# Optimization experiments

Measured on AMD Instinct MI355X. Metric: run time of the kernel, lower is better.

Reference implementation:

```python
import jax, jax.numpy as jnp
import numpy as np

B = 32          # decode batch
H = 32          # query heads (TP shard)
KV_LORA = 512   # latent dim
ROPE = 64       # rope head dim
NOPE = 128      # nope head dim
VH = 128        # v head dim
QL = 1536       # q lora rank
HID = 5120      # model hidden
BLK = 128       # page/block size
BLOCKS_PER_SEQ = 32   # 4096-token context
NB = B * BLOCKS_PER_SEQ
CACHE_BLOCKS = 1200


def _rope(x, pos):
    # x: [B, n, ROPE] (neox half-rotation), pos: [B] int positions
    half = x.shape[-1] // 2
    inv = 1.0 / (10000.0 ** (jnp.arange(half, dtype=jnp.float32) / half))
    ang = pos.astype(jnp.float32)[:, None] * inv              # [B, half]
    cos, sin = jnp.cos(ang)[:, None, :], jnp.sin(ang)[:, None, :]
    x1, x2 = x[..., :half], x[..., half:]
    return jnp.concatenate([x1 * cos - x2 * sin, x2 * cos + x1 * sin], axis=-1)


def setup_inputs() -> dict:
    key = jax.random.key(0)
    ks = jax.random.split(key, 10)
    inp = {
        'hidden_states_or_q_c': jax.random.normal(ks[0], (B, QL), jnp.float32),
        'k_c_normed': jax.random.normal(ks[1], (B, 1, KV_LORA), jnp.float32),
        'k_pe': jax.random.normal(ks[2], (B, 1, ROPE), jnp.float32),
        'kv_cache_k': jax.random.normal(ks[3], (CACHE_BLOCKS, BLK, ROPE), jnp.float32),
        'kv_cache_v': jax.random.normal(ks[4], (CACHE_BLOCKS, BLK, KV_LORA), jnp.float32),
        'W_Q': jax.random.normal(ks[5], (QL, H * NOPE), jnp.float32) / np.sqrt(QL),
        'W_UK': jax.random.normal(ks[6], (H, NOPE, KV_LORA), jnp.float32) / np.sqrt(NOPE),
        'W_QR': jax.random.normal(ks[7], (QL, H * ROPE), jnp.float32) / np.sqrt(QL),
        'W_UV': jax.random.normal(ks[8], (H, KV_LORA, VH), jnp.float32) / np.sqrt(KV_LORA),
        'W_O': jax.random.normal(ks[9], (H * VH, HID), jnp.float32) / np.sqrt(H * VH),
        'input_positions': jnp.full((B,), BLK * BLOCKS_PER_SEQ - 1, jnp.int32),
        'block_list': jnp.arange(NB, dtype=jnp.int32),
        'block_groups': (jnp.arange(NB, dtype=jnp.int32) // BLOCKS_PER_SEQ),
        'block_bias': jnp.zeros((NB, BLK), jnp.float32),
        'block_indices': (jnp.arange(B, dtype=jnp.int32) * BLOCKS_PER_SEQ + BLOCKS_PER_SEQ - 1),
        'block_offsets': jnp.full((B,), BLK - 1, jnp.int32),
    }
    inp['block_mapping'] = jax.nn.one_hot(inp['block_groups'], B, dtype=jnp.float32)
    return inp


def reference(hidden_states_or_q_c, k_c_normed, k_pe, kv_cache_k, kv_cache_v,
              W_Q, W_UK, W_QR, W_UV, W_O,
              input_positions, block_list, block_groups, block_mapping,
              block_bias, block_indices, block_offsets):
    b = hidden_states_or_q_c.shape[0]
    h, nope, kv_lora = W_UK.shape
    rope = k_pe.shape[-1]
    scale = 1.0 / np.sqrt(nope + rope)

    # absorbed q projection: q_nope in latent space (_q_proj_and_k_up_proj)
    q_nope = jnp.einsum('bq,qhd->bhd', hidden_states_or_q_c, W_Q.reshape(-1, h, nope))
    q_nope = jnp.einsum('bhd,hdl->bhl', q_nope, W_UK)          # [B,H,kv_lora]
    q_pe = (hidden_states_or_q_c @ W_QR).reshape(b, h, rope)
    pos = input_positions.reshape(b)
    q_pe = _rope(q_pe, pos)
    k_pe_r = _rope(k_pe, pos)                                  # [B,1,rope]

    # write new latent token into paged cache (latent_cache_k / latent_cache_v)
    kv_cache_k = kv_cache_k.at[block_indices, block_offsets].set(k_pe_r[:, 0, :])
    kv_cache_v = kv_cache_v.at[block_indices, block_offsets].set(k_c_normed[:, 0, :])

    # flat_pa_mla: query [B,H,kv_lora+rope], key = concat(value_latent, k_pe)
    q = jnp.concatenate([q_nope, q_pe], axis=-1) * scale       # [B,H,576]
    keys = kv_cache_k[block_list]                              # [NB,BLK,rope]
    vals = kv_cache_v[block_list]                              # [NB,BLK,kv_lora]
    kcat = jnp.concatenate([vals, keys], axis=-1)              # [NB,BLK,576]

    qb = jnp.einsum('nb,bhd->nhd', block_mapping, q)           # batch2block
    logits = jnp.einsum('nhd,nkd->nhk', qb, kcat) + block_bias[:, None, :]

    # grouped (per-batch) softmax across this batch's blocks == pipelined_pa math
    gmax = jax.ops.segment_max(logits.max(-1), block_groups, num_segments=b)  # [B,H]
    p = jnp.exp(logits - gmax[block_groups][:, :, None])       # [NB,H,BLK]
    av = jnp.einsum('nhk,nkl->nhl', p, vals)                   # [NB,H,kv_lora]
    num = jnp.einsum('nb,nhl->bhl', block_mapping, av)         # block2batch
    den = jnp.einsum('nb,nh->bh', block_mapping, p.sum(-1))
    attn = num / den[..., None]                                # [B,H,kv_lora]

    # _v_up_proj_and_o_proj
    out = jnp.einsum('bhl,hlv->bhv', attn, W_UV).reshape(b, -1) @ W_O
    return out.reshape(b, 1, -1)
```

## Files before the change

kernel.cpp:

```cpp
#include <hip/hip_runtime.h>
#include <hip/hip_bf16.h>
#include <stdint.h>


typedef __attribute__((ext_vector_type(8))) short short8;
typedef __attribute__((ext_vector_type(4))) float f32x4;

__device__ inline uint32_t f2bf(float f) {
  uint32_t u = __float_as_uint(f);
  return (u + 0x7fffu + ((u >> 16) & 1u)) >> 16;
}
union Bf2U { __hip_bfloat162 h; uint32_t u; };
__device__ inline uint32_t pack2bf(float lo, float hi) {
  Bf2U v; v.h = __float22bfloat162_rn(float2{lo, hi});
  return v.u;
}
union FragU { uint32_t u[4]; short8 s; };
__device__ inline short8 frag_from(const uint32_t r[4]) {
  FragU v; v.u[0] = r[0]; v.u[1] = r[1]; v.u[2] = r[2]; v.u[3] = r[3];
  return v.s;
}

__global__ __launch_bounds__(256) void k1_qproj(
    const float* __restrict__ hidden, const float* __restrict__ W_Q,
    const float* __restrict__ W_QR, float* __restrict__ q_nope0,
    float* __restrict__ q_pe0) {
  __shared__ float hl[32][129];
  const int t = threadIdx.x;
  const int ctile = blockIdx.x * 128;
  const int k0 = blockIdx.y * 128;
  const bool isQ = (ctile < 4096);
  const float* W = isQ ? W_Q : W_QR;
  const int wstride = isQ ? 4096 : 2048;
  const int c = (isQ ? ctile : ctile - 4096) + (t & 31) * 4;
  const int rg = t >> 5;
  for (int idx = t; idx < 4096; idx += 256) {
    int b = idx >> 7, kk = idx & 127;
    hl[b][kk] = hidden[b * 1536 + k0 + kk];
  }
  __syncthreads();
  float acc[4][4];
#pragma unroll
  for (int r = 0; r < 4; ++r)
#pragma unroll
    for (int j = 0; j < 4; ++j) acc[r][j] = 0.f;
  const float* wp = W + (size_t)k0 * wstride + c;
#pragma unroll 4
  for (int kk = 0; kk < 128; ++kk) {
    float4 w = *(const float4*)wp;
    wp += wstride;
#pragma unroll
    for (int r = 0; r < 4; ++r) {
      float hv = hl[rg * 4 + r][kk];
      acc[r][0] += hv * w.x;
      acc[r][1] += hv * w.y;
      acc[r][2] += hv * w.z;
      acc[r][3] += hv * w.w;
    }
  }
  float* dst = isQ ? q_nope0 : q_pe0;
#pragma unroll
  for (int r = 0; r < 4; ++r)
#pragma unroll
    for (int j = 0; j < 4; ++j)
      atomicAdd(&dst[(rg * 4 + r) * wstride + c + j], acc[r][j]);
}

__global__ __launch_bounds__(256) void k2_qlora(
    const float* __restrict__ q_nope0, const float* __restrict__ W_UK,
    float* __restrict__ q_acc) {
  __shared__ float qn[32][33];
  const int t = threadIdx.x;
  const int h = blockIdx.y;
  const int c0 = blockIdx.x * 128;
  const int d0 = blockIdx.z * 32;
  for (int idx = t; idx < 1024; idx += 256) {
    int b = idx >> 5, dd = idx & 31;
    qn[b][dd] = q_nope0[b * 4096 + h * 128 + d0 + dd];
  }
  __syncthreads();
  const int c = c0 + (t & 31) * 4;
  const int rg = t >> 5;
  float acc[4][4];
#pragma unroll
  for (int r = 0; r < 4; ++r)
#pragma unroll
    for (int j = 0; j < 4; ++j) acc[r][j] = 0.f;
  const float* wp = W_UK + (size_t)(h * 128 + d0) * 512 + c;
#pragma unroll 4
  for (int dd = 0; dd < 32; ++dd) {
    float4 w = *(const float4*)wp;
    wp += 512;
#pragma unroll
    for (int r = 0; r < 4; ++r) {
      float qv = qn[rg * 4 + r][dd];
      acc[r][0] += qv * w.x;
      acc[r][1] += qv * w.y;
      acc[r][2] += qv * w.z;
      acc[r][3] += qv * w.w;
    }
  }
#pragma unroll
  for (int r = 0; r < 4; ++r)
#pragma unroll
    for (int j = 0; j < 4; ++j)
      atomicAdd(&q_acc[(size_t)((rg * 4 + r) * 32 + h) * 512 + c + j],
                acc[r][j]);
}

__global__ __launch_bounds__(256) void k2b_rope_scatter(
    const float* __restrict__ q_pe0, const float* __restrict__ k_pe,
    const float* __restrict__ k_c_normed, const int* __restrict__ ipos,
    const int* __restrict__ bindices, const int* __restrict__ boffsets,
    const float* __restrict__ q_acc, float* __restrict__ cache_k,
    float* __restrict__ cache_v, uint16_t* __restrict__ q_bf) {
  const int b = blockIdx.x;
  const int hs = blockIdx.y * 4;
  const int t = threadIdx.x;
  const float pos = (float)ipos[b];
  const float scale = 0.07216878364870323f;
  const float lnk = 0.28782313662425575f;
  for (int idx = t; idx < 2048; idx += 256) {
    int h = hs + (idx >> 9), c = idx & 511;
    q_bf[((size_t)b * 32 + h) * 576 + c] =
        (uint16_t)f2bf(q_acc[((size_t)b * 32 + h) * 512 + c] * scale);
  }
  if (t < 128) {
    int h = hs + (t >> 5), i = t & 31;
    float ang = pos * __expf(-(float)i * lnk);
    float s, c;
    sincosf(ang, &s, &c);
    float x1 = q_pe0[b * 2048 + h * 64 + i];
    float x2 = q_pe0[b * 2048 + h * 64 + 32 + i];
    int base = (b * 32 + h) * 576 + 512;
    q_bf[base + i]      = (uint16_t)f2bf((x1 * c - x2 * s) * scale);
    q_bf[base + 32 + i] = (uint16_t)f2bf((x2 * c + x1 * s) * scale);
  }
  if (blockIdx.y == 0) {
    const int row = bindices[b] * 128 + boffsets[b];
    if (t < 32) {
      int i = t;
      float ang = pos * __expf(-(float)i * lnk);
      float s, c;
      sincosf(ang, &s, &c);
      float x1 = k_pe[b * 64 + i], x2 = k_pe[b * 64 + 32 + i];
      cache_k[row * 64 + i]      = x1 * c - x2 * s;
      cache_k[row * 64 + 32 + i] = x2 * c + x1 * s;
    }
    for (int j = t; j < 512; j += 256)
      cache_v[row * 512 + j] = k_c_normed[b * 512 + j];
  }
}

__global__ __launch_bounds__(256, 2) void k3_attn(
    const uint16_t* __restrict__ q_bf, const float* __restrict__ cache_k,
    const float* __restrict__ cache_v, const int* __restrict__ block_list,
    const int* __restrict__ block_groups, const float* __restrict__ block_bias,
    float* __restrict__ num_part, float* __restrict__ den_part) {
  __shared__ uint32_t Tl[288 * 33];
  __shared__ uint32_t Pl[16 * 33];
  __shared__ float den_sh[2][32];

  const int t = threadIdx.x;
  const int part = blockIdx.x, bseq = blockIdx.y;
  const int wg = bseq * 16 + part;
  const int wave = t >> 6, lane = t & 63, quad = lane >> 4, l16 = lane & 15;
  const int hh = wave >> 1, kvh = wave & 1;
  const int n0 = bseq * 32 + part * 2;
  const int g = block_groups[n0];

  uint32_t qf[72];
  {
    const uint32_t* qrow =
        (const uint32_t*)(q_bf + (size_t)(g * 32 + hh * 16 + l16) * 576);
#pragma unroll
    for (int ks = 0; ks < 18; ++ks)
#pragma unroll
      for (int i = 0; i < 4; ++i)
        qf[ks * 4 + i] = qrow[ks * 16 + quad * 4 + i];
  }

  const f32x4 fzero = {0.f, 0.f, 0.f, 0.f};
  f32x4 acc[2][8];
#pragma unroll
  for (int mt = 0; mt < 2; ++mt)
#pragma unroll
    for (int nt = 0; nt < 8; ++nt) acc[mt][nt] = fzero;
  float den_acc[4] = {0.f, 0.f, 0.f, 0.f};

  for (int blk_i = 0; blk_i < 2; ++blk_i) {
    const int n = n0 + blk_i;
    const int phys = block_list[n];
    const float* vrow = cache_v + (size_t)phys * 128 * 512;
    const float* krow = cache_k + (size_t)phys * 128 * 64;
    for (int s = 0; s < 4; ++s) {
      const int s0 = s * 32;
      __syncthreads();
      for (int idx = t; idx < 4608; idx += 256) {
        int kv = idx / 144, f4 = idx - kv * 144;
        float4 v; int d0;
        if (f4 < 128) { v = *(const float4*)(vrow + (s0 + kv) * 512 + f4 * 4); d0 = f4 * 4; }
        else { v = *(const float4*)(krow + (s0 + kv) * 64 + (f4 - 128) * 4); d0 = 512 + (f4 - 128) * 4; }
        int d2 = d0 >> 1;
        Tl[(d2    ) * 33 + kv] = pack2bf(v.x, v.y);
        Tl[(d2 + 1) * 33 + kv] = pack2bf(v.z, v.w);
      }
      __syncthreads();
      const int tkv = kvh * 16 + l16;
      f32x4 lg = fzero;
#pragma unroll
      for (int ks = 0; ks < 18; ++ks) {
        uint32_t br[4];
#pragma unroll
        for (int i = 0; i < 4; ++i)
          br[i] = Tl[(ks * 16 + quad * 4 + i) * 33 + tkv];
        lg = __builtin_amdgcn_mfma_f32_16x16x32_bf16(
            frag_from(&qf[ks * 4]), frag_from(br), lg, 0, 0, 0);
      }
      float bias = block_bias[n * 128 + s0 + tkv];
      uint32_t pb[4];
#pragma unroll
      for (int r = 0; r < 4; ++r) {
        float p = __expf(lg[r] + bias);
        pb[r] = f2bf(p);
        den_acc[r] += __uint_as_float(pb[r] << 16);
      }
#pragma unroll
      for (int r = 0; r < 4; ++r) {
        uint32_t other = (uint32_t)__shfl_xor((int)pb[r], 1, 64);
        if ((l16 & 1) == 0) {
          int h = hh * 16 + quad * 4 + r;
          Pl[(tkv >> 1) * 33 + h] = pb[r] | (other << 16);
        }
      }
      __syncthreads();
      uint32_t af[2][4];
#pragma unroll
      for (int mt = 0; mt < 2; ++mt)
#pragma unroll
        for (int i = 0; i < 4; ++i)
          af[mt][i] = Pl[(quad * 4 + i) * 33 + mt * 16 + l16];
#pragma unroll
      for (int nt = 0; nt < 8; ++nt) {
        int l = wave * 128 + nt * 16 + l16;
        const uint32_t* base = &Tl[(l >> 1) * 33 + quad * 8];
        uint32_t dw[8];
#pragma unroll
        for (int j = 0; j < 8; ++j) dw[j] = base[j];
        uint32_t br[4];
        const bool odd = (l & 1);
#pragma unroll
        for (int i = 0; i < 4; ++i) {
          uint32_t a = dw[2 * i], bq = dw[2 * i + 1];
          uint32_t lo = odd ? (a >> 16) : (a & 0xffffu);
          uint32_t hi = odd ? (bq & 0xffff0000u) : (bq << 16);
          br[i] = lo | hi;
        }
        short8 bf = frag_from(br);
        acc[0][nt] = __builtin_amdgcn_mfma_f32_16x16x32_bf16(
            frag_from(af[0]), bf, acc[0][nt], 0, 0, 0);
        acc[1][nt] = __builtin_amdgcn_mfma_f32_16x16x32_bf16(
            frag_from(af[1]), bf, acc[1][nt], 0, 0, 0);
      }
    }
  }
#pragma unroll
  for (int mt = 0; mt < 2; ++mt)
#pragma unroll
    for (int nt = 0; nt < 8; ++nt)
#pragma unroll
      for (int r = 0; r < 4; ++r) {
        int h = mt * 16 + quad * 4 + r;
        int l = wave * 128 + nt * 16 + l16;
        num_part[((size_t)wg * 32 + h) * 512 + l] = acc[mt][nt][r];
      }
  float dv[4];
#pragma unroll
  for (int r = 0; r < 4; ++r) {
    float v = den_acc[r];
    v += __shfl_xor(v, 1, 64);
    v += __shfl_xor(v, 2, 64);
    v += __shfl_xor(v, 4, 64);
    v += __shfl_xor(v, 8, 64);
    dv[r] = v;
  }
  if (l16 == 0) {
#pragma unroll
    for (int r = 0; r < 4; ++r)
      den_sh[kvh][hh * 16 + quad * 4 + r] = dv[r];
  }
  __syncthreads();
  if (t < 32) den_part[wg * 32 + t] = den_sh[0][t] + den_sh[1][t];
}

__global__ __launch_bounds__(256) void k4_reduce_wuv(
    const float* __restrict__ num_part, const float* __restrict__ den_part,
    const float* __restrict__ W_UV, float* __restrict__ o_acc) {
  __shared__ float attn[32][33];
  __shared__ float den[32];
  const int t = threadIdx.x;
  const int lc = blockIdx.x, h = blockIdx.y;
  const int c0 = lc * 32;
  if (t < 32) {
    float s = 0.f;
    for (int p = 0; p < 16; ++p) s += den_part[(t * 16 + p) * 32 + h];
    den[t] = s;
  }
  __syncthreads();
  {
    const int b = t >> 3, l4 = (t & 7) * 4;
    float4 s = {0.f, 0.f, 0.f, 0.f};
#pragma unroll
    for (int p = 0; p < 16; ++p) {
      float4 v = *(const float4*)&num_part[((size_t)(b * 16 + p) * 32 + h) * 512 + c0 + l4];
      s.x += v.x; s.y += v.y; s.z += v.z; s.w += v.w;
    }
    float inv = 1.f / den[b];
    attn[b][l4 + 0] = s.x * inv;
    attn[b][l4 + 1] = s.y * inv;
    attn[b][l4 + 2] = s.z * inv;
    attn[b][l4 + 3] = s.w * inv;
  }
  __syncthreads();
  const int v = t & 127, rg = t >> 7;
  float acc[16];
#pragma unroll
  for (int r = 0; r < 16; ++r) acc[r] = 0.f;
  for (int l = 0; l < 32; ++l) {
    float w = W_UV[(h * 512 + c0 + l) * 128 + v];
#pragma unroll
    for (int r = 0; r < 16; ++r) acc[r] += attn[rg * 16 + r][l] * w;
  }
  for (int r = 0; r < 16; ++r)
    atomicAdd(&o_acc[(size_t)(rg * 16 + r) * 4096 + h * 128 + v], acc[r]);
}

__global__ __launch_bounds__(256) void k5_wo(
    const float* __restrict__ o_acc, const float* __restrict__ W_O,
    float* __restrict__ out) {
  __shared__ uint32_t Bt[32 * 130];
  const int t = threadIdx.x;
  const int ksplit = blockIdx.x, ntile = blockIdx.y;
  const int n0 = ntile * 128, kbase = ksplit * 256;
  const int wave = t >> 6, lane = t & 63, quad = lane >> 4, l16 = lane & 15;
  const f32x4 fzero = {0.f, 0.f, 0.f, 0.f};
  f32x4 acc[2][2];
#pragma unroll
  for (int mt = 0; mt < 2; ++mt)
#pragma unroll
    for (int nt = 0; nt < 2; ++nt) acc[mt][nt] = fzero;
  for (int kc = 0; kc < 4; ++kc) {
    const int k0 = kbase + kc * 64;
    __syncthreads();
    for (int idx = t; idx < 1024; idx += 256) {
      int k2 = idx >> 5, c4 = idx & 31;
      const float* p0 = &W_O[(size_t)(k0 + 2 * k2) * 5120 + n0 + c4 * 4];
      float4 a = *(const float4*)p0;
      float4 b = *(const float4*)(p0 + 5120);
      uint32_t* bp = &Bt[k2 * 130 + c4 * 4];
      bp[0] = pack2bf(a.x, b.x);
      bp[1] = pack2bf(a.y, b.y);
      bp[2] = pack2bf(a.z, b.z);
      bp[3] = pack2bf(a.w, b.w);
    }
    __syncthreads();
#pragma unroll
    for (int ks2 = 0; ks2 < 2; ++ks2) {
      uint32_t af[2][4];
#pragma unroll
      for (int mt = 0; mt < 2; ++mt) {
        const float* orow =
            o_acc + (size_t)(mt * 16 + l16) * 4096 + k0 + ks2 * 32 + quad * 8;
        float4 x = *(const float4*)orow;
        float4 y = *(const float4*)(orow + 4);
        af[mt][0] = pack2bf(x.x, x.y);
        af[mt][1] = pack2bf(x.z, x.w);
        af[mt][2] = pack2bf(y.x, y.y);
        af[mt][3] = pack2bf(y.z, y.w);
      }
#pragma unroll
      for (int nt = 0; nt < 2; ++nt) {
        uint32_t br[4];
#pragma unroll
        for (int i = 0; i < 4; ++i)
          br[i] = Bt[(ks2 * 16 + quad * 4 + i) * 130 + wave * 32 + nt * 16 + l16];
        short8 bf = frag_from(br);
        acc[0][nt] = __builtin_amdgcn_mfma_f32_16x16x32_bf16(
            frag_from(af[0]), bf, acc[0][nt], 0, 0, 0);
        acc[1][nt] = __builtin_amdgcn_mfma_f32_16x16x32_bf16(
            frag_from(af[1]), bf, acc[1][nt], 0, 0, 0);
      }
    }
  }
#pragma unroll
  for (int mt = 0; mt < 2; ++mt)
#pragma unroll
    for (int nt = 0; nt < 2; ++nt)
#pragma unroll
      for (int r = 0; r < 4; ++r) {
        int b = mt * 16 + quad * 4 + r;
        int c = n0 + wave * 32 + nt * 16 + l16;
        atomicAdd(&out[(size_t)b * 5120 + c], acc[mt][nt][r]);
      }
}

extern "C" void kernel_launch(void* const* d_in, const int* in_sizes, int n_in,
                              void* d_out, int out_size, void* d_ws,
                              size_t ws_size, hipStream_t stream) {
  (void)in_sizes; (void)n_in; (void)ws_size;
  const float* hidden = (const float*)d_in[0];
  const float* k_c    = (const float*)d_in[1];
  const float* k_pe   = (const float*)d_in[2];
  float* cache_k      = (float*)d_in[3];
  float* cache_v      = (float*)d_in[4];
  const float* W_Q    = (const float*)d_in[5];
  const float* W_UK   = (const float*)d_in[6];
  const float* W_QR   = (const float*)d_in[7];
  const float* W_UV   = (const float*)d_in[8];
  const float* W_O    = (const float*)d_in[9];
  const int* ipos     = (const int*)d_in[10];
  const int* blist    = (const int*)d_in[11];
  const int* bgroups  = (const int*)d_in[12];
  const float* bbias  = (const float*)d_in[13];
  const int* bindices = (const int*)d_in[14];
  const int* boffsets = (const int*)d_in[15];

  char* ws = (char*)d_ws;
  float*    q_nope0  = (float*)(ws);
  float*    q_pe0    = (float*)(ws + 524288);
  float*    o_acc    = (float*)(ws + 786432);
  uint16_t* q_bf     = (uint16_t*)(ws + 1310720);
  float*    den_part = (float*)(ws + 2490368);
  float*    num_part = (float*)(ws + 2555904);
  float*    q_acc    = num_part;
  float*    out      = (float*)d_out;

  hipMemsetAsync(ws, 0, 1310720, stream);
  hipMemsetAsync((void*)q_acc, 0, 2097152, stream);
  hipMemsetAsync(d_out, 0, (size_t)out_size * sizeof(float), stream);

  k1_qproj<<<dim3(48, 12), 256, 0, stream>>>(hidden, W_Q, W_QR, q_nope0, q_pe0);
  k2_qlora<<<dim3(4, 32, 4), 256, 0, stream>>>(q_nope0, W_UK, q_acc);
  k2b_rope_scatter<<<dim3(32, 8), 256, 0, stream>>>(q_pe0, k_pe, k_c, ipos,
                                                    bindices, boffsets, q_acc,
                                                    cache_k, cache_v, q_bf);
  k3_attn<<<dim3(16, 32), 256, 0, stream>>>(q_bf, cache_k, cache_v, blist,
                                            bgroups, bbias, num_part, den_part);
  k4_reduce_wuv<<<dim3(16, 32), 256, 0, stream>>>(num_part, den_part, W_UV, o_acc);
  k5_wo<<<dim3(16, 40), 256, 0, stream>>>(o_acc, W_O, out);
}
```

Baseline: 702.4 us.

## Reduce attention partials with atomics and split cache tile loads

The attention kernel now adds its per-block numerator and denominator directly into per-sequence accumulators with atomicAdd, instead of writing 16 partials per sequence for the reduce kernel to sum. The reduce kernel only normalizes and applies W_UV, using 64-column tiles over half as many workgroups. The cache tile load loop is split into separate unrolled V and K loops, which removes the per-element branch and the division by 144. In exchange there is a larger memset, contention on the float atomics, and a floating-point summation order that is no longer deterministic.

```diff
diff --git a/kernel.cpp b/kernel.cpp
--- a/kernel.cpp
+++ b/kernel.cpp
@@ -156,14 +156,13 @@
     const uint16_t* __restrict__ q_bf, const float* __restrict__ cache_k,
     const float* __restrict__ cache_v, const int* __restrict__ block_list,
     const int* __restrict__ block_groups, const float* __restrict__ block_bias,
-    float* __restrict__ num_part, float* __restrict__ den_part) {
+    float* __restrict__ num_acc, float* __restrict__ den_acc) {
   __shared__ uint32_t Tl[288 * 33];
   __shared__ uint32_t Pl[16 * 33];
   __shared__ float den_sh[2][32];
 
   const int t = threadIdx.x;
   const int part = blockIdx.x, bseq = blockIdx.y;
-  const int wg = bseq * 16 + part;
   const int wave = t >> 6, lane = t & 63, quad = lane >> 4, l16 = lane & 15;
   const int hh = wave >> 1, kvh = wave & 1;
   const int n0 = bseq * 32 + part * 2;
@@ -186,7 +185,7 @@
   for (int mt = 0; mt < 2; ++mt)
 #pragma unroll
     for (int nt = 0; nt < 8; ++nt) acc[mt][nt] = fzero;
-  float den_acc[4] = {0.f, 0.f, 0.f, 0.f};
+  float den_acc_r[4] = {0.f, 0.f, 0.f, 0.f};
 
   for (int blk_i = 0; blk_i < 2; ++blk_i) {
     const int n = n0 + blk_i;
@@ -196,12 +195,21 @@
     for (int s = 0; s < 4; ++s) {
       const int s0 = s * 32;
       __syncthreads();
-      for (int idx = t; idx < 4608; idx += 256) {
-        int kv = idx / 144, f4 = idx - kv * 144;
-        float4 v; int d0;
-        if (f4 < 128) { v = *(const float4*)(vrow + (s0 + kv) * 512 + f4 * 4); d0 = f4 * 4; }
-        else { v = *(const float4*)(krow + (s0 + kv) * 64 + (f4 - 128) * 4); d0 = 512 + (f4 - 128) * 4; }
-        int d2 = d0 >> 1;
+#pragma unroll
+      for (int i = 0; i < 16; ++i) {
+        int idx = i * 256 + t;
+        int kv = idx >> 7, f4 = idx & 127;
+        float4 v = *(const float4*)(vrow + (s0 + kv) * 512 + f4 * 4);
+        int d2 = f4 * 2;
+        Tl[(d2    ) * 33 + kv] = pack2bf(v.x, v.y);
+        Tl[(d2 + 1) * 33 + kv] = pack2bf(v.z, v.w);
+      }
+#pragma unroll
+      for (int i = 0; i < 2; ++i) {
+        int idx = i * 256 + t;
+        int kv = idx >> 4, f4 = idx & 15;
+        float4 v = *(const float4*)(krow + (s0 + kv) * 64 + f4 * 4);
+        int d2 = 256 + f4 * 2;
         Tl[(d2    ) * 33 + kv] = pack2bf(v.x, v.y);
         Tl[(d2 + 1) * 33 + kv] = pack2bf(v.z, v.w);
       }
@@ -223,7 +231,7 @@
       for (int r = 0; r < 4; ++r) {
         float p = __expf(lg[r] + bias);
         pb[r] = f2bf(p);
-        den_acc[r] += __uint_as_float(pb[r] << 16);
+        den_acc_r[r] += __uint_as_float(pb[r] << 16);
       }
 #pragma unroll
       for (int r = 0; r < 4; ++r) {
@@ -272,12 +280,12 @@
       for (int r = 0; r < 4; ++r) {
         int h = mt * 16 + quad * 4 + r;
         int l = wave * 128 + nt * 16 + l16;
-        num_part[((size_t)wg * 32 + h) * 512 + l] = acc[mt][nt][r];
+        atomicAdd(&num_acc[((size_t)(g * 32 + h)) * 512 + l], acc[mt][nt][r]);
       }
   float dv[4];
 #pragma unroll
   for (int r = 0; r < 4; ++r) {
-    float v = den_acc[r];
+    float v = den_acc_r[r];
     v += __shfl_xor(v, 1, 64);
     v += __shfl_xor(v, 2, 64);
     v += __shfl_xor(v, 4, 64);
@@ -290,47 +298,37 @@
       den_sh[kvh][hh * 16 + quad * 4 + r] = dv[r];
   }
   __syncthreads();
-  if (t < 32) den_part[wg * 32 + t] = den_sh[0][t] + den_sh[1][t];
+  if (t < 32) atomicAdd(&den_acc[g * 32 + t], den_sh[0][t] + den_sh[1][t]);
 }
 
 __global__ __launch_bounds__(256) void k4_reduce_wuv(
-    const float* __restrict__ num_part, const float* __restrict__ den_part,
+    const float* __restrict__ num_acc, const float* __restrict__ den_acc,
     const float* __restrict__ W_UV, float* __restrict__ o_acc) {
-  __shared__ float attn[32][33];
-  __shared__ float den[32];
-  const int t = threadIdx.x;
-  const int lc = blockIdx.x, h = blockIdx.y;
-  const int c0 = lc * 32;
-  if (t < 32) {
-    float s = 0.f;
-    for (int p = 0; p < 16; ++p) s += den_part[(t * 16 + p) * 32 + h];
-    den[t] = s;
-  }
+  __shared__ float attn[32][65];
+  __shared__ float inv[32];
+  const int t = threadIdx.x;
+  const int l0 = blockIdx.x * 64;
+  const int h = blockIdx.y;
+  if (t < 32) inv[t] = 1.f / den_acc[t * 32 + h];
   __syncthreads();
-  {
-    const int b = t >> 3, l4 = (t & 7) * 4;
-    float4 s = {0.f, 0.f, 0.f, 0.f};
-#pragma unroll
-    for (int p = 0; p < 16; ++p) {
-      float4 v = *(const float4*)&num_part[((size_t)(b * 16 + p) * 32 + h) * 512 + c0 + l4];
-      s.x += v.x; s.y += v.y; s.z += v.z; s.w += v.w;
-    }
-    float inv = 1.f / den[b];
-    attn[b][l4 + 0] = s.x * inv;
-    attn[b][l4 + 1] = s.y * inv;
-    attn[b][l4 + 2] = s.z * inv;
-    attn[b][l4 + 3] = s.w * inv;
+  for (int idx = t; idx < 2048; idx += 256) {
+    int b = idx >> 6, l = idx & 63;
+    attn[b][l] = num_acc[((size_t)(b * 32 + h)) * 512 + l0 + l] * inv[b];
   }
   __syncthreads();
   const int v = t & 127, rg = t >> 7;
   float acc[16];
 #pragma unroll
   for (int r = 0; r < 16; ++r) acc[r] = 0.f;
-  for (int l = 0; l < 32; ++l) {
-    float w = W_UV[(h * 512 + c0 + l) * 128 + v];
+  const float* wp = W_UV + ((size_t)h * 512 + l0) * 128 + v;
+#pragma unroll 4
+  for (int l = 0; l < 64; ++l) {
+    float w = *wp;
+    wp += 128;
 #pragma unroll
     for (int r = 0; r < 16; ++r) acc[r] += attn[rg * 16 + r][l] * w;
   }
+#pragma unroll
   for (int r = 0; r < 16; ++r)
     atomicAdd(&o_acc[(size_t)(rg * 16 + r) * 4096 + h * 128 + v], acc[r]);
 }
@@ -429,14 +427,13 @@
   float*    q_nope0  = (float*)(ws);
   float*    q_pe0    = (float*)(ws + 524288);
   float*    o_acc    = (float*)(ws + 786432);
-  uint16_t* q_bf     = (uint16_t*)(ws + 1310720);
-  float*    den_part = (float*)(ws + 2490368);
-  float*    num_part = (float*)(ws + 2555904);
-  float*    q_acc    = num_part;
+  float*    q_acc    = (float*)(ws + 1310720);
+  float*    num_acc  = (float*)(ws + 3407872);
+  float*    den_acc  = (float*)(ws + 7602176);
+  uint16_t* q_bf     = (uint16_t*)(ws + 7606272);
   float*    out      = (float*)d_out;
 
-  hipMemsetAsync(ws, 0, 1310720, stream);
-  hipMemsetAsync((void*)q_acc, 0, 2097152, stream);
+  hipMemsetAsync(ws, 0, 7606272, stream);
   hipMemsetAsync(d_out, 0, (size_t)out_size * sizeof(float), stream);
 
   k1_qproj<<<dim3(48, 12), 256, 0, stream>>>(hidden, W_Q, W_QR, q_nope0, q_pe0);
@@ -445,7 +442,7 @@
                                                     bindices, boffsets, q_acc,
                                                     cache_k, cache_v, q_bf);
   k3_attn<<<dim3(16, 32), 256, 0, stream>>>(q_bf, cache_k, cache_v, blist,
-                                            bgroups, bbias, num_part, den_part);
-  k4_reduce_wuv<<<dim3(16, 32), 256, 0, stream>>>(num_part, den_part, W_UV, o_acc);
+                                            bgroups, bbias, num_acc, den_acc);
+  k4_reduce_wuv<<<dim3(8, 32), 256, 0, stream>>>(num_acc, den_acc, W_UV, o_acc);
   k5_wo<<<dim3(16, 40), 256, 0, stream>>>(o_acc, W_O, out);
 }
```

Measured after the change: 693.2 us. Within noise of the previous version (-1.3%).
